# Kernel optimization log

Measured on AMD Instinct MI355X. Metric: run time of the kernel, lower is better.

Reference implementation:

```python
import jax, jax.numpy as jnp
import numpy as np

B, D, H, O = 8192, 1024, 2048, 1024   # batch, input_dim, hidden_dim, output_dim
T, NOPS = 4, 3                        # num_tempers, operators per bank (fixed at init)


def setup_inputs() -> dict:
    key = jax.random.key(0)
    ks = jax.random.split(key, 6)
    sc = 0.02
    return {
        "x": jax.random.normal(ks[0], (B, D), jnp.float32),
        # per-temper input_proj: Linear(D -> H)
        "Wp": jax.random.normal(ks[1], (T, H, D), jnp.float32) * sc,
        "bp": jnp.zeros((T, H), jnp.float32),
        "Wop": jax.random.normal(ks[2], (T, NOPS, H, H), jnp.float32) * sc,
        "bop": jnp.zeros((T, NOPS, H), jnp.float32),
        # routing_logits ~ randn per Temper.__init__
        "logits": jax.random.normal(ks[3], (T, NOPS), jnp.float32),
        # readout: Linear(T*H -> O)
        "Wr": jax.random.normal(ks[4], (O, T * H), jnp.float32) * sc,
        "br": jnp.zeros((O,), jnp.float32),
    }


def reference(x, Wp, bp, Wop, bop, logits, Wr, br):
    def temper(Wp_i, bp_i, Wop_i, bop_i, lg):
        # input projection: [B, H]
        xp = x @ Wp_i.T + bp_i
        # top-2 routing over operator bank (output is unweighted dispatch)
        w = jax.nn.softmax(lg)
        _, idx = jax.lax.top_k(w, 2)
        Wa, ba = Wop_i[idx[0]], bop_i[idx[0]]
        Wb, bb = Wop_i[idx[1]], bop_i[idx[1]]
        # each operator = Sequential(ReLU, Linear, ReLU)
        h = jax.nn.relu(jax.nn.relu(xp) @ Wa.T + ba)
        return jax.nn.relu(jax.nn.relu(h) @ Wb.T + bb)

    outs = jax.vmap(temper)(Wp, bp, Wop, bop, logits)          # [T, B, H]
    cat = jnp.transpose(outs, (1, 0, 2)).reshape(x.shape[0], -1)  # [B, T*H]
    return cat @ Wr.T + br                                      # [B, O]
```

## Files before the change

### kernel.cpp

```cpp
#include <hip/hip_runtime.h>

static constexpr int Bn = 8192;
static constexpr int Dd = 1024;
static constexpr int Hh = 2048;
static constexpr int Oo = 1024;
static constexpr int Tt = 4;
static constexpr int NO = 3;
#define TB 256

typedef __attribute__((ext_vector_type(8))) short bf16x8;
typedef __attribute__((ext_vector_type(4))) float f32x4;

__device__ __forceinline__ ushort f2bf(float f) {
  union { float f; unsigned u; } v; v.f = f;
  return (ushort)((v.u + 0x7FFFu + ((v.u >> 16) & 1u)) >> 16);
}

__global__ void top2_kernel(const float* __restrict__ logits, int* __restrict__ idx) {
  if (threadIdx.x == 0 && blockIdx.x == 0) {
    for (int t = 0; t < Tt; ++t) {
      const float* lg = logits + t * NO;
      int i0 = 0;
      for (int k = 1; k < NO; ++k) if (lg[k] > lg[i0]) i0 = k;
      int i1 = -1;
      for (int k = 0; k < NO; ++k) {
        if (k == i0) continue;
        if (i1 < 0 || lg[k] > lg[i1]) i1 = k;
      }
      idx[2 * t] = i0;
      idx[2 * t + 1] = i1;
    }
  }
}

__global__ void cvt_bf16(const float* __restrict__ src, ushort* __restrict__ dst, int n4) {
  int i = blockIdx.x * blockDim.x + threadIdx.x;
  if (i >= n4) return;
  float4 v = ((const float4*)src)[i];
  ((ushort4*)dst)[i] = make_ushort4(f2bf(v.x), f2bf(v.y), f2bf(v.z), f2bf(v.w));
}

__global__ void cvt_sel(const float* __restrict__ WopT, const int* __restrict__ idx2,
                        ushort* __restrict__ Wa, ushort* __restrict__ Wb, int n4) {
  int i = blockIdx.x * blockDim.x + threadIdx.x;
  if (i >= n4) return;
  size_t n = (size_t)n4 * 4;
  float4 va = ((const float4*)(WopT + (size_t)idx2[0] * n))[i];
  float4 vb = ((const float4*)(WopT + (size_t)idx2[1] * n))[i];
  ((ushort4*)Wa)[i] = make_ushort4(f2bf(va.x), f2bf(va.y), f2bf(va.z), f2bf(va.w));
  ((ushort4*)Wb)[i] = make_ushort4(f2bf(vb.x), f2bf(vb.y), f2bf(vb.z), f2bf(vb.w));
}

#define ISSUE_TILE(kk, p)                                                                   \
  do {                                                                                      \
    __builtin_amdgcn_global_load_lds(                                                       \
        (const __attribute__((address_space(1))) void*)(a0 + (kk)),                         \
        (__attribute__((address_space(3))) void*)(&As[p][w * 512]), 16, 0, 0);              \
    __builtin_amdgcn_global_load_lds(                                                       \
        (const __attribute__((address_space(1))) void*)(a1 + (kk)),                         \
        (__attribute__((address_space(3))) void*)(&As[p][2048 + w * 512]), 16, 0, 0);       \
    __builtin_amdgcn_global_load_lds(                                                       \
        (const __attribute__((address_space(1))) void*)(b0 + (kk)),                         \
        (__attribute__((address_space(3))) void*)(&Bs[p][w * 512]), 16, 0, 0);              \
    __builtin_amdgcn_global_load_lds(                                                       \
        (const __attribute__((address_space(1))) void*)(b1 + (kk)),                         \
        (__attribute__((address_space(3))) void*)(&Bs[p][2048 + w * 512]), 16, 0, 0);       \
  } while (0)

template <int EP>
__global__ __launch_bounds__(TB) void gemm_bt(
    const ushort* __restrict__ A, int lda,
    const ushort* __restrict__ B, int ldb,
    const float* __restrict__ bias, const int* __restrict__ idxp, int sel, int bstride,
    void* __restrict__ Cv, int ldc, int K) {
  __shared__ __align__(16) ushort As[2][128 * 32];
  __shared__ __align__(16) ushort Bs[2][128 * 32];
  const int tid = threadIdx.x;
  const int w = tid >> 6;
  const int lane = tid & 63;
  const int quad = lane >> 4;
  const int l16 = lane & 15;

  const int GX = gridDim.x, GY = gridDim.y;
  const int f = blockIdx.y * GX + blockIdx.x;
  const int xcd = f & 7;
  const int s = f >> 3;
  const int pxc = (GX >= 16) ? 2 : 1;
  const int pw = GX / pxc;
  const int ph = (GY * pxc) >> 3;
  const int bx = (xcd % pxc) * pw + (s % pw);
  const int by = (xcd / pxc) * ph + (s / pw);
  const int m0 = by * 128;
  const int n0 = bx * 128;
  const int wm = (w >> 1) * 64;
  const int wn = (w & 1) * 64;

  f32x4 acc[4][4];
#pragma unroll
  for (int i = 0; i < 4; ++i)
#pragma unroll
    for (int j = 0; j < 4; ++j)
#pragma unroll
      for (int r = 0; r < 4; ++r) acc[i][j][r] = 0.f;

  const int srow = tid >> 2;
  const int skc = ((tid & 3) ^ ((tid >> 3) & 3)) * 8;
  const ushort* a0 = A + (size_t)(m0 + srow) * lda + skc;
  const ushort* a1 = A + (size_t)(m0 + 64 + srow) * lda + skc;
  const ushort* b0 = B + (size_t)(n0 + srow) * ldb + skc;
  const ushort* b1 = B + (size_t)(n0 + 64 + srow) * ldb + skc;

  const int fq = (quad ^ ((l16 >> 1) & 3)) * 8;

  const int niter = K >> 5;
  ISSUE_TILE(0, 0);
  for (int it = 0; it < niter; ++it) {
    const int p = it & 1;
    __syncthreads();
    if (it + 1 < niter) ISSUE_TILE((it + 1) << 5, p ^ 1);

    bf16x8 af[4], bfr[4];
#pragma unroll
    for (int i = 0; i < 4; ++i)
      af[i] = *(const bf16x8*)&As[p][((wm >> 4) + i) * 512 + l16 * 32 + fq];
#pragma unroll
    for (int j = 0; j < 4; ++j)
      bfr[j] = *(const bf16x8*)&Bs[p][((wn >> 4) + j) * 512 + l16 * 32 + fq];
#pragma unroll
    for (int i = 0; i < 4; ++i)
#pragma unroll
      for (int j = 0; j < 4; ++j)
        acc[i][j] = __builtin_amdgcn_mfma_f32_16x16x32_bf16(af[i], bfr[j], acc[i][j], 0, 0, 0);
  }

  const float* bb = bias;
  if (EP == 0 && idxp) bb += (size_t)idxp[sel] * bstride;

#pragma unroll
  for (int i = 0; i < 4; ++i) {
#pragma unroll
    for (int j = 0; j < 4; ++j) {
      const int col = n0 + wn + j * 16 + l16;
      const float bv = (EP == 2) ? 0.f : bb[col];
#pragma unroll
      for (int r = 0; r < 4; ++r) {
        const int row = m0 + wm + i * 16 + quad * 4 + r;
        float v = acc[i][j][r] + bv;
        if (EP == 0) {
          v = v > 0.f ? v : 0.f;
          ((ushort*)Cv)[(size_t)row * ldc + col] = f2bf(v);
        } else if (EP == 1) {
          ((float*)Cv)[(size_t)row * ldc + col] = v;
        } else {
          ((float*)Cv)[(size_t)row * ldc + col] += v;
        }
      }
    }
  }
}

#define BAR() __builtin_amdgcn_s_barrier()
#define SCHEDB() __builtin_amdgcn_sched_barrier(0)
#define WAITLGKM() asm volatile("s_waitcnt lgkmcnt(0)" ::: "memory")
#define WAITVM(N) asm volatile("s_waitcnt vmcnt(" #N ")" ::: "memory")

#define STG(BASE, LD, ARR, P, H, KT)                                                        \
  do {                                                                                      \
    const int kt_ = ((KT) < ntile) ? (KT) : (ntile - 1);                                    \
    const ushort* g_ = (BASE) + (size_t)(H) * 128 * (LD) + (size_t)kt_ * 64;                \
    __builtin_amdgcn_global_load_lds(                                                       \
        (const __attribute__((address_space(1))) void*)g_,                                  \
        (__attribute__((address_space(3))) void*)&ARR[(P) * 16384 + (H) * 8192 + w * 512],  \
        16, 0, 0);                                                                          \
    __builtin_amdgcn_global_load_lds(                                                       \
        (const __attribute__((address_space(1))) void*)(g_ + (size_t)64 * (LD)),            \
        (__attribute__((address_space(3))) void*)&ARR[(P) * 16384 + (H) * 8192 + 4096 +     \
                                                      w * 512],                             \
        16, 0, 0);                                                                          \
  } while (0)

#define RD_A(P, MH)                                                                         \
  do {                                                                                      \
    _Pragma("unroll") for (int mf = 0; mf < 4; ++mf)                                        \
    _Pragma("unroll") for (int kk = 0; kk < 2; ++kk)                                        \
        af[mf][kk] = *(const bf16x8*)&As[(P) * 16384 + ak[kk] + ((MH) * 4 + mf) * 1024];    \
  } while (0)

#define RD_B(P, NH)                                                                         \
  do {                                                                                      \
    _Pragma("unroll") for (int nf = 0; nf < 2; ++nf)                                        \
    _Pragma("unroll") for (int kk = 0; kk < 2; ++kk)                                        \
        bfr[(NH) * 2 + nf][kk] =                                                            \
            *(const bf16x8*)&Bs[(P) * 16384 + bk[kk] + ((NH) * 2 + nf) * 1024];             \
  } while (0)

#define MFMA_Q(MH, NH)                                                                      \
  do {                                                                                      \
    __builtin_amdgcn_s_setprio(1);                                                          \
    _Pragma("unroll") for (int mf = 0; mf < 4; ++mf)                                        \
    _Pragma("unroll") for (int nf = 0; nf < 2; ++nf)                                        \
    _Pragma("unroll") for (int kk = 0; kk < 2; ++kk)                                        \
        acc[(MH) * 4 + mf][(NH) * 2 + nf] = __builtin_amdgcn_mfma_f32_16x16x32_bf16(        \
            af[mf][kk], bfr[(NH) * 2 + nf][kk], acc[(MH) * 4 + mf][(NH) * 2 + nf], 0, 0, 0);\
    __builtin_amdgcn_s_setprio(0);                                                          \
  } while (0)

template <int EP>
__global__ __launch_bounds__(512, 2) void gemm256(
    const ushort* __restrict__ A, int lda,
    const ushort* __restrict__ B, int ldb,
    const float* __restrict__ bias, const int* __restrict__ idxp, int sel, int bstride,
    void* __restrict__ Cv, int ldc, int K) {
  __shared__ __align__(16) ushort As[32768];
  __shared__ __align__(16) ushort Bs[32768];
  const int tid = threadIdx.x;
  const int w = tid >> 6;
  const int lane = tid & 63;
  const int quad = lane >> 4;
  const int l16 = lane & 15;
  const int wr = w >> 2;
  const int wc = w & 3;

  const int GX = gridDim.x;
  const int nwg = GX * gridDim.y;
  const int fid = blockIdx.y * GX + blockIdx.x;
  const int q8 = nwg >> 3, r8 = nwg & 7, xcd = fid & 7, ser = fid >> 3;
  const int wg = (xcd < r8 ? xcd * (q8 + 1) : r8 * (q8 + 1) + (xcd - r8) * q8) + ser;
  const int m0 = (wg / GX) * 256;
  const int n0 = (wg % GX) * 256;

  f32x4 acc[8][4];
#pragma unroll
  for (int i = 0; i < 8; ++i)
#pragma unroll
    for (int j = 0; j < 4; ++j)
#pragma unroll
      for (int r = 0; r < 4; ++r) acc[i][j][r] = 0.f;

  const int srow = tid >> 3;
  const int scol = (tid & 7) ^ (srow & 7);
  const ushort* Abase = A + (size_t)(m0 + srow) * lda + scol * 8;
  const ushort* Bbase = B + (size_t)(n0 + srow) * ldb + scol * 8;
  const int ntile = K >> 6;
  const int ni = ntile >> 1;

  int ak[2], bk[2];
#pragma unroll
  for (int kk = 0; kk < 2; ++kk) {
    const int ch = ((kk * 4 + quad) ^ (l16 & 7)) * 8;
    ak[kk] = wr * 8192 + l16 * 64 + ch;
    bk[kk] = (wc >> 1) * 8192 + ((wc & 1) * 64 + l16) * 64 + ch;
  }

  STG(Abase, lda, As, 0, 0, 0);
  STG(Abase, lda, As, 0, 1, 0);
  STG(Bbase, ldb, Bs, 0, 0, 0);
  STG(Bbase, ldb, Bs, 0, 1, 0);
  STG(Bbase, ldb, Bs, 1, 0, 1);
  STG(Bbase, ldb, Bs, 1, 1, 1);
  WAITVM(4);
  BAR();
  SCHEDB();

  bf16x8 af[4][2], bfr[4][2];
  for (int i = 0; i < ni; ++i) {
    const int t = 2 * i;
    RD_A(0, 0); RD_B(0, 0);
    STG(Abase, lda, As, 1, 0, t + 1);
    BAR(); WAITLGKM();
    MFMA_Q(0, 0);
    BAR();
    RD_B(0, 1);
    STG(Abase, lda, As, 1, 1, t + 1);
    BAR(); WAITLGKM();
    MFMA_Q(0, 1);
    BAR();
    RD_A(0, 1);
    STG(Bbase, ldb, Bs, 0, 0, t + 2);
    BAR(); WAITLGKM();
    MFMA_Q(1, 0);
    BAR();
    STG(Bbase, ldb, Bs, 0, 1, t + 2);
    WAITVM(4);
    BAR();
    SCHEDB();
    MFMA_Q(1, 1);
    BAR();
    RD_A(1, 0); RD_B(1, 0);
    STG(Abase, lda, As, 0, 0, t + 2);
    BAR(); WAITLGKM();
    MFMA_Q(0, 0);
    BAR();
    RD_B(1, 1);
    STG(Abase, lda, As, 0, 1, t + 2);
    BAR(); WAITLGKM();
    MFMA_Q(0, 1);
    BAR();
    RD_A(1, 1);
    STG(Bbase, ldb, Bs, 1, 0, t + 3);
    BAR(); WAITLGKM();
    MFMA_Q(1, 0);
    BAR();
    STG(Bbase, ldb, Bs, 1, 1, t + 3);
    WAITVM(4);
    BAR();
    SCHEDB();
    MFMA_Q(1, 1);
    BAR();
  }
  WAITVM(0);
  BAR();

  const float* bb = bias;
  if (EP == 0 && idxp) bb += (size_t)idxp[sel] * bstride;

#pragma unroll
  for (int mf = 0; mf < 8; ++mf) {
#pragma unroll
    for (int nf = 0; nf < 4; ++nf) {
      const int col = n0 + wc * 64 + nf * 16 + l16;
      const float bv = (EP == 2) ? 0.f : bb[col];
#pragma unroll
      for (int r = 0; r < 4; ++r) {
        const int row = m0 + wr * 128 + mf * 16 + quad * 4 + r;
        float v = acc[mf][nf][r] + bv;
        if (EP == 0) {
          v = v > 0.f ? v : 0.f;
          ((ushort*)Cv)[(size_t)row * ldc + col] = f2bf(v);
        } else if (EP == 1) {
          ((float*)Cv)[(size_t)row * ldc + col] = v;
        } else {
          ((float*)Cv)[(size_t)row * ldc + col] += v;
        }
      }
    }
  }
}

extern "C" void kernel_launch(void* const* d_in, const int* in_sizes, int n_in,
                              void* d_out, int out_size, void* d_ws, size_t ws_size,
                              hipStream_t stream) {
  const float* x      = (const float*)d_in[0];
  const float* Wp     = (const float*)d_in[1];
  const float* bp     = (const float*)d_in[2];
  const float* Wop    = (const float*)d_in[3];
  const float* bop    = (const float*)d_in[4];
  const float* logits = (const float*)d_in[5];
  const float* Wr     = (const float*)d_in[6];
  const float* br     = (const float*)d_in[7];
  float* out = (float*)d_out;

  char* ws = (char*)d_ws;
  size_t off = 0;
  int* idx = (int*)ws;                          off += 256;
  ushort* xb   = (ushort*)(ws + off);           off += (size_t)Bn * Dd * 2;
  ushort* WpB  = (ushort*)(ws + off);           off += (size_t)Tt * Hh * Dd * 2;
  ushort* WrB  = (ushort*)(ws + off);           off += (size_t)Oo * Tt * Hh * 2;
  ushort* WaB  = (ushort*)(ws + off);           off += (size_t)Hh * Hh * 2;
  ushort* WbB  = (ushort*)(ws + off);           off += (size_t)Hh * Hh * 2;
  ushort* bufA = (ushort*)(ws + off);           off += (size_t)Bn * Hh * 2;
  ushort* bufB = (ushort*)(ws + off);           off += (size_t)Bn * Hh * 2;

  top2_kernel<<<1, 64, 0, stream>>>(logits, idx);
  {
    int n4 = Bn * Dd / 4;
    cvt_bf16<<<(n4 + TB - 1) / TB, TB, 0, stream>>>(x, xb, n4);
  }
  {
    int n4 = Tt * Hh * Dd / 4;
    cvt_bf16<<<(n4 + TB - 1) / TB, TB, 0, stream>>>(Wp, WpB, n4);
  }
  {
    int n4 = Oo * Tt * Hh / 4;
    cvt_bf16<<<(n4 + TB - 1) / TB, TB, 0, stream>>>(Wr, WrB, n4);
  }

  dim3 g256(Hh / 256, Bn / 256);
  dim3 gOB(Oo / 128, Bn / 128);

  for (int t = 0; t < Tt; ++t) {
    int n4 = Hh * Hh / 4;
    cvt_sel<<<(n4 + TB - 1) / TB, TB, 0, stream>>>(Wop + (size_t)t * NO * Hh * Hh, idx + 2 * t,
                                                   WaB, WbB, n4);
    gemm256<0><<<g256, 512, 0, stream>>>(xb, Dd, WpB + (size_t)t * Hh * Dd, Dd,
                                         bp + (size_t)t * Hh, nullptr, 0, 0, bufA, Hh, Dd);
    gemm256<0><<<g256, 512, 0, stream>>>(bufA, Hh, WaB, Hh,
                                         bop + (size_t)t * NO * Hh, idx + 2 * t, 0, Hh,
                                         bufB, Hh, Hh);
    gemm256<0><<<g256, 512, 0, stream>>>(bufB, Hh, WbB, Hh,
                                         bop + (size_t)t * NO * Hh, idx + 2 * t, 1, Hh,
                                         bufA, Hh, Hh);
    if (t == 0)
      gemm_bt<1><<<gOB, TB, 0, stream>>>(bufA, Hh, WrB + (size_t)t * Hh, Tt * Hh,
                                         br, nullptr, 0, 0, out, Oo, Hh);
    else
      gemm_bt<2><<<gOB, TB, 0, stream>>>(bufA, Hh, WrB + (size_t)t * Hh, Tt * Hh,
                                         nullptr, nullptr, 0, 0, out, Oo, Hh);
  }
}
```

Measured before the change: 1.216 ms.

## Batch all tempers into wide and batched GEMMs with split-K readout

When the workspace is large enough, the four per-temper chains are replaced by a few large launches. One GEMM produces all input projections (N = 4*2048). Two batched GEMMs over a z-dimension of tempers apply the two selected operators, and the readout runs as a single split-K GEMM with two halves followed by an elementwise add. The goal is to cut launch count, expose more workgroups per launch and fill the GPU better, replacing the small 128-tile readout kernel with the 256-tile one. The cost is larger intermediate buffers, an extra fp32 partial-output buffer and an add pass. The old per-temper path is kept as a fallback.

Measured after the change: 1.197 ms. No clear change (-1.6%).

```diff
diff --git a/kernel.cpp b/kernel.cpp
--- a/kernel.cpp
+++ b/kernel.cpp
@@ -6,6 +6,7 @@
 static constexpr int Oo = 1024;
 static constexpr int Tt = 4;
 static constexpr int NO = 3;
+static constexpr int TH = Tt * Hh;
 #define TB 256
 
 typedef __attribute__((ext_vector_type(8))) short bf16x8;
@@ -51,6 +52,28 @@
   ((ushort4*)Wb)[i] = make_ushort4(f2bf(vb.x), f2bf(vb.y), f2bf(vb.z), f2bf(vb.w));
 }
 
+__global__ void cvt_sel8(const float* __restrict__ Wop, const int* __restrict__ idx,
+                         ushort* __restrict__ W8, int n4) {
+  int i = blockIdx.x * blockDim.x + threadIdx.x;
+  if (i >= n4) return;
+  int z = blockIdx.z;
+  int t = z >> 1, slot = z & 1;
+  int op = idx[2 * t + slot];
+  const float4* src = (const float4*)(Wop + ((size_t)t * NO + op) * Hh * Hh);
+  float4 v = src[i];
+  ((ushort4*)(W8 + (size_t)z * Hh * Hh))[i] =
+      make_ushort4(f2bf(v.x), f2bf(v.y), f2bf(v.z), f2bf(v.w));
+}
+
+__global__ void add_f32(float* __restrict__ out, const float* __restrict__ p1, int n4) {
+  int i = blockIdx.x * blockDim.x + threadIdx.x;
+  if (i >= n4) return;
+  float4 a = ((const float4*)out)[i];
+  float4 b = ((const float4*)p1)[i];
+  a.x += b.x; a.y += b.y; a.z += b.z; a.w += b.w;
+  ((float4*)out)[i] = a;
+}
+
 #define ISSUE_TILE(kk, p)                                                                   \
   do {                                                                                      \
     __builtin_amdgcn_global_load_lds(                                                       \
@@ -141,7 +164,7 @@
 #pragma unroll
     for (int j = 0; j < 4; ++j) {
       const int col = n0 + wn + j * 16 + l16;
-      const float bv = (EP == 2) ? 0.f : bb[col];
+      const float bv = (EP == 2 || !bias) ? 0.f : bb[col];
 #pragma unroll
       for (int r = 0; r < 4; ++r) {
         const int row = m0 + wm + i * 16 + quad * 4 + r;
@@ -207,10 +230,12 @@
 
 template <int EP>
 __global__ __launch_bounds__(512, 2) void gemm256(
-    const ushort* __restrict__ A, int lda,
-    const ushort* __restrict__ B, int ldb,
-    const float* __restrict__ bias, const int* __restrict__ idxp, int sel, int bstride,
-    void* __restrict__ Cv, int ldc, int K) {
+    const ushort* __restrict__ A, int lda, long az,
+    const ushort* __restrict__ B, int ldb, long bz,
+    const float* __restrict__ bias, long bias_zstride,
+    const int* __restrict__ idxp, int sel0, int sel_zmul, int bstride,
+    void* __restrict__ Cv, int ldc, long cz, float* __restrict__ C1,
+    int K) {
   __shared__ __align__(16) ushort As[32768];
   __shared__ __align__(16) ushort Bs[32768];
   const int tid = threadIdx.x;
@@ -220,6 +245,10 @@
   const int l16 = lane & 15;
   const int wr = w >> 2;
   const int wc = w & 3;
+  const int z = blockIdx.z;
+
+  A += (size_t)z * az;
+  B += (size_t)z * bz;
 
   const int GX = gridDim.x;
   const int nwg = GX * gridDim.y;
@@ -312,25 +341,31 @@
   BAR();
 
   const float* bb = bias;
-  if (EP == 0 && idxp) bb += (size_t)idxp[sel] * bstride;
+  if (bias) {
+    bb += (size_t)z * bias_zstride;
+    if (idxp) bb += (size_t)idxp[sel0 + z * sel_zmul] * bstride;
+  }
+  const bool nobias = (EP != 0) && (bias == nullptr || (z != 0 && C1 != nullptr));
+  ushort* Cu = (EP == 0) ? (ushort*)Cv + (size_t)z * cz : nullptr;
+  float* Cf = (EP == 0) ? nullptr : ((EP == 1 && z != 0 && C1) ? C1 : (float*)Cv);
 
 #pragma unroll
   for (int mf = 0; mf < 8; ++mf) {
 #pragma unroll
     for (int nf = 0; nf < 4; ++nf) {
       const int col = n0 + wc * 64 + nf * 16 + l16;
-      const float bv = (EP == 2) ? 0.f : bb[col];
+      const float bv = (EP == 2 || nobias) ? 0.f : bb[col];
 #pragma unroll
       for (int r = 0; r < 4; ++r) {
         const int row = m0 + wr * 128 + mf * 16 + quad * 4 + r;
         float v = acc[mf][nf][r] + bv;
         if (EP == 0) {
           v = v > 0.f ? v : 0.f;
-          ((ushort*)Cv)[(size_t)row * ldc + col] = f2bf(v);
+          Cu[(size_t)row * ldc + col] = f2bf(v);
         } else if (EP == 1) {
-          ((float*)Cv)[(size_t)row * ldc + col] = v;
+          Cf[(size_t)row * ldc + col] = v;
         } else {
-          ((float*)Cv)[(size_t)row * ldc + col] += v;
+          Cf[(size_t)row * ldc + col] += v;
         }
       }
     }
@@ -350,16 +385,15 @@
   const float* br     = (const float*)d_in[7];
   float* out = (float*)d_out;
 
+  const size_t MB = 1024 * 1024;
+  const size_t need_fused = 256 + (size_t)(16 + 16 + 16 + 64 + 128 + 128 + 32) * MB;
+
   char* ws = (char*)d_ws;
   size_t off = 0;
   int* idx = (int*)ws;                          off += 256;
   ushort* xb   = (ushort*)(ws + off);           off += (size_t)Bn * Dd * 2;
   ushort* WpB  = (ushort*)(ws + off);           off += (size_t)Tt * Hh * Dd * 2;
-  ushort* WrB  = (ushort*)(ws + off);           off += (size_t)Oo * Tt * Hh * 2;
-  ushort* WaB  = (ushort*)(ws + off);           off += (size_t)Hh * Hh * 2;
-  ushort* WbB  = (ushort*)(ws + off);           off += (size_t)Hh * Hh * 2;
-  ushort* bufA = (ushort*)(ws + off);           off += (size_t)Bn * Hh * 2;
-  ushort* bufB = (ushort*)(ws + off);           off += (size_t)Bn * Hh * 2;
+  ushort* WrB  = (ushort*)(ws + off);           off += (size_t)Oo * TH * 2;
 
   top2_kernel<<<1, 64, 0, stream>>>(logits, idx);
   {
@@ -371,30 +405,68 @@
     cvt_bf16<<<(n4 + TB - 1) / TB, TB, 0, stream>>>(Wp, WpB, n4);
   }
   {
-    int n4 = Oo * Tt * Hh / 4;
+    int n4 = Oo * TH / 4;
     cvt_bf16<<<(n4 + TB - 1) / TB, TB, 0, stream>>>(Wr, WrB, n4);
   }
 
-  dim3 g256(Hh / 256, Bn / 256);
-  dim3 gOB(Oo / 128, Bn / 128);
-
-  for (int t = 0; t < Tt; ++t) {
-    int n4 = Hh * Hh / 4;
-    cvt_sel<<<(n4 + TB - 1) / TB, TB, 0, stream>>>(Wop + (size_t)t * NO * Hh * Hh, idx + 2 * t,
-                                                   WaB, WbB, n4);
-    gemm256<0><<<g256, 512, 0, stream>>>(xb, Dd, WpB + (size_t)t * Hh * Dd, Dd,
-                                         bp + (size_t)t * Hh, nullptr, 0, 0, bufA, Hh, Dd);
-    gemm256<0><<<g256, 512, 0, stream>>>(bufA, Hh, WaB, Hh,
-                                         bop + (size_t)t * NO * Hh, idx + 2 * t, 0, Hh,
-                                         bufB, Hh, Hh);
-    gemm256<0><<<g256, 512, 0, stream>>>(bufB, Hh, WbB, Hh,
-                                         bop + (size_t)t * NO * Hh, idx + 2 * t, 1, Hh,
-                                         bufA, Hh, Hh);
-    if (t == 0)
-      gemm_bt<1><<<gOB, TB, 0, stream>>>(bufA, Hh, WrB + (size_t)t * Hh, Tt * Hh,
-                                         br, nullptr, 0, 0, out, Oo, Hh);
-    else
-      gemm_bt<2><<<gOB, TB, 0, stream>>>(bufA, Hh, WrB + (size_t)t * Hh, Tt * Hh,
-                                         nullptr, nullptr, 0, 0, out, Oo, Hh);
-  }
-}
+  if (ws_size >= need_fused) {
+    ushort* W8    = (ushort*)(ws + off);        off += (size_t)8 * Hh * Hh * 2;
+    ushort* xpcat = (ushort*)(ws + off);        off += (size_t)Bn * TH * 2;
+    ushort* hcat  = (ushort*)(ws + off);        off += (size_t)Bn * TH * 2;
+    float*  out1  = (float*)(ws + off);         off += (size_t)Bn * Oo * 4;
+
+    {
+      int n4 = Hh * Hh / 4;
+      dim3 g((n4 + TB - 1) / TB, 1, 8);
+      cvt_sel8<<<g, TB, 0, stream>>>(Wop, idx, W8, n4);
+    }
+
+    gemm256<0><<<dim3(TH / 256, Bn / 256, 1), 512, 0, stream>>>(
+        xb, Dd, 0, WpB, Dd, 0, bp, 0, nullptr, 0, 0, 0, xpcat, TH, 0, nullptr, Dd);
+
+    gemm256<0><<<dim3(Hh / 256, Bn / 256, Tt), 512, 0, stream>>>(
+        xpcat, TH, Hh, W8, Hh, (long)2 * Hh * Hh,
+        bop, (long)NO * Hh, idx, 0, 2, Hh, hcat, TH, Hh, nullptr, Hh);
+
+    gemm256<0><<<dim3(Hh / 256, Bn / 256, Tt), 512, 0, stream>>>(
+        hcat, TH, Hh, W8 + (size_t)Hh * Hh, Hh, (long)2 * Hh * Hh,
+        bop, (long)NO * Hh, idx, 1, 2, Hh, xpcat, TH, Hh, nullptr, Hh);
+
+    gemm256<1><<<dim3(Oo / 256, Bn / 256, 2), 512, 0, stream>>>(
+        xpcat, TH, (long)TH / 2, WrB, TH, (long)TH / 2,
+        br, 0, nullptr, 0, 0, 0, out, Oo, 0, out1, TH / 2);
+    {
+      int n4 = Bn * Oo / 4;
+      add_f32<<<(n4 + TB - 1) / TB, TB, 0, stream>>>(out, out1, n4);
+    }
+  } else {
+    ushort* WaB  = (ushort*)(ws + off);         off += (size_t)Hh * Hh * 2;
+    ushort* WbB  = (ushort*)(ws + off);         off += (size_t)Hh * Hh * 2;
+    ushort* bufA = (ushort*)(ws + off);         off += (size_t)Bn * Hh * 2;
+    ushort* bufB = (ushort*)(ws + off);         off += (size_t)Bn * Hh * 2;
+
+    dim3 g256(Hh / 256, Bn / 256);
+    dim3 gOB(Oo / 128, Bn / 128);
+
+    for (int t = 0; t < Tt; ++t) {
+      int n4 = Hh * Hh / 4;
+      cvt_sel<<<(n4 + TB - 1) / TB, TB, 0, stream>>>(Wop + (size_t)t * NO * Hh * Hh,
+                                                     idx + 2 * t, WaB, WbB, n4);
+      gemm256<0><<<g256, 512, 0, stream>>>(
+          xb, Dd, 0, WpB + (size_t)t * Hh * Dd, Dd, 0,
+          bp + (size_t)t * Hh, 0, nullptr, 0, 0, 0, bufA, Hh, 0, nullptr, Dd);
+      gemm256<0><<<g256, 512, 0, stream>>>(
+          bufA, Hh, 0, WaB, Hh, 0,
+          bop + (size_t)t * NO * Hh, 0, idx, 2 * t, 0, Hh, bufB, Hh, 0, nullptr, Hh);
+      gemm256<0><<<g256, 512, 0, stream>>>(
+          bufB, Hh, 0, WbB, Hh, 0,
+          bop + (size_t)t * NO * Hh, 0, idx, 2 * t + 1, 0, Hh, bufA, Hh, 0, nullptr, Hh);
+      if (t == 0)
+        gemm_bt<1><<<gOB, TB, 0, stream>>>(bufA, Hh, WrB + (size_t)t * Hh, TH,
+                                           br, nullptr, 0, 0, out, Oo, Hh);
+      else
+        gemm_bt<2><<<gOB, TB, 0, stream>>>(bufA, Hh, WrB + (size_t)t * Hh, TH,
+                                           nullptr, nullptr, 0, 0, out, Oo, Hh);
+    }
+  }
+}
```
